# Kernel optimization log

Measured on AMD Instinct MI355X. Metric: run time of the kernel, lower is better.

## Reference

```python
import jax, jax.numpy as jnp
import numpy as np
import math

B, HO, WO, MO, NID, NOBJ = 8, 152, 272, 128, 537, 64
EMB_SCALE = math.sqrt(2.0) * math.log(NID - 1)

# ---------- host-side target construction (faithful CenterNet/FairMOT assignment) ----------

def gaussian_radius(det_size, min_overlap=0.7):
    height, width = det_size
    b1 = height + width
    c1 = width * height * (1 - min_overlap) / (1 + min_overlap)
    r1 = (b1 + math.sqrt(max(b1 * b1 - 4 * c1, 0.0))) / 2
    b2 = 2 * (height + width)
    c2 = (1 - min_overlap) * width * height
    r2 = (b2 + math.sqrt(max(b2 * b2 - 16 * c2, 0.0))) / 2
    a3 = 4 * min_overlap
    b3 = -2 * min_overlap * (height + width)
    c3 = (min_overlap - 1) * width * height
    r3 = (b3 + math.sqrt(max(b3 * b3 - 4 * a3 * c3, 0.0))) / 2
    return min(r1, r2, r3)

def gaussian2D(shape, sigma=1.0):
    m, n = [(s - 1.0) / 2.0 for s in shape]
    y, x = np.ogrid[-m:m + 1, -n:n + 1]
    h = np.exp(-(x * x + y * y) / (2 * sigma * sigma))
    h[h < np.finfo(h.dtype).eps * h.max()] = 0
    return h

def draw_umich_gaussian(heatmap, center, radius, k=1):
    diameter = 2 * radius + 1
    gaussian = gaussian2D((diameter, diameter), sigma=diameter / 6.0)
    x, y = int(center[0]), int(center[1])
    height, width = heatmap.shape
    left, right = min(x, radius), min(width - x, radius + 1)
    top, bottom = min(y, radius), min(height - y, radius + 1)
    mh = heatmap[y - top:y + bottom, x - left:x + right]
    mg = gaussian[radius - top:radius + bottom, radius - left:radius + right]
    if min(mg.shape) > 0 and min(mh.shape) > 0:
        np.maximum(mh, mg * k, out=mh)


def setup_inputs() -> dict:
    rng = np.random.default_rng(0)
    hm = np.zeros((B, 1, HO, WO), np.float32)
    wh = np.zeros((B, MO, 8), np.float32)
    v = np.zeros((B, MO), np.float32)
    ind = np.zeros((B, MO), np.int64)
    reg_mask = np.zeros((B, MO), np.int32)
    ids = np.zeros((B, MO), np.int64)
    for b in range(B):
        cx = rng.uniform(0.1, 0.9, NOBJ); cy = rng.uniform(0.1, 0.9, NOBJ)
        bw = rng.uniform(0.02, 0.15, NOBJ); bh = rng.uniform(0.05, 0.3, NOBJ)
        pid = rng.choice(NID, NOBJ, replace=False)
        vis = rng.uniform(0.3, 1.0, NOBJ)
        cx2 = np.clip(cx + rng.normal(0, 0.01, NOBJ), 0.05, 0.95)
        cy2 = np.clip(cy + rng.normal(0, 0.01, NOBJ), 0.05, 0.95)
        bw2 = bw * rng.uniform(0.9, 1.1, NOBJ); bh2 = bh * rng.uniform(0.9, 1.1, NOBJ)
        for k in range(NOBJ):
            x, y, w_, h_ = cx[k] * WO, cy[k] * HO, bw[k] * WO, bh[k] * HO
            ax0, ay0 = x - w_ / 2.0, y - h_ / 2.0
            ax1, ay1 = ax0 + w_, ay0 + h_
            xc, yc = float(np.clip(x, 0, WO - 1)), float(np.clip(y, 0, HO - 1))
            r = max(0, int(gaussian_radius((math.ceil(h_), math.ceil(w_)))))
            ctx, cty = int(xc), int(yc)
            draw_umich_gaussian(hm[b, 0], (ctx, cty), r)
            x2, y2, w2_, h2_ = cx2[k] * WO, cy2[k] * HO, bw2[k] * WO, bh2[k] * HO
            bx0, by0 = x2 - w2_ / 2.0, y2 - h2_ / 2.0
            bx1, by1 = bx0 + w2_, by0 + h2_
            if h_ > 0 and w_ > 0 and h2_ > 0 and w2_ > 0:
                ind[b, k] = cty * WO + ctx
                wh[b, k] = (ctx - ax0, ax1 - ctx, cty - ay0, ay1 - cty,
                            ctx - bx0, bx1 - ctx, cty - by0, by1 - cty)
                reg_mask[b, k] = 1
                ids[b, k] = pid[k]
                v[b, k] = vis[k]
    key = jax.random.key(0)
    ks = jax.random.split(key, 14)
    mk = lambda i, s: jax.random.normal(ks[i], s, dtype=jnp.float32)
    return {
        'classifications': mk(0, (B, 1, HO, WO)),
        'regressions': mk(1, (B, 8, HO, WO)),
        'viss': mk(2, (B, 1, HO, WO)),
        'identis_64': mk(3, (B, 64, HO, WO)),
        'identis_128': mk(4, (B, 128, HO, WO)),
        'identis_256': mk(5, (B, 256, HO, WO)),
        'identis_end': mk(6, (B, 128, HO, WO)),
        'hm': jnp.asarray(hm), 'wh': jnp.asarray(wh), 'v': jnp.asarray(v),
        'W64': mk(7, (NID, 64)) * 0.02, 'b64': jnp.zeros((NID,), jnp.float32),
        'W128': mk(8, (NID, 128)) * 0.02, 'b128': jnp.zeros((NID,), jnp.float32),
        'W256': mk(9, (NID, 256)) * 0.02, 'b256': jnp.zeros((NID,), jnp.float32),
        'Wend': mk(10, (NID, 128)) * 0.02, 'bend': jnp.zeros((NID,), jnp.float32),
        's_det': mk(11, (1,)), 's_id': mk(12, (1,)),
        'ind': jnp.asarray(ind), 'reg_mask': jnp.asarray(reg_mask), 'ids': jnp.asarray(ids),
    }

# ---------- jax loss math ----------

def _gather(feat, ind):
    # feat: [B,C,H,W] -> gathered [B,MO,C]
    b, c = feat.shape[0], feat.shape[1]
    f = feat.reshape(b, c, -1).transpose(0, 2, 1)  # [B,HW,C]
    return jnp.take_along_axis(f, ind[:, :, None], axis=1)


def _focal(pred, gt):
    # CenterNet focal loss, per image
    pos = (gt == 1.0).astype(pred.dtype)
    neg_w = (1.0 - gt) ** 4
    pos_l = jnp.log(pred) * (1.0 - pred) ** 2 * pos
    neg_l = jnp.log(1.0 - pred) * pred ** 2 * neg_w * (1.0 - pos)
    npos = pos.sum(axis=(1, 2, 3))
    pl, nl = pos_l.sum(axis=(1, 2, 3)), neg_l.sum(axis=(1, 2, 3))
    return jnp.where(npos > 0, -(pl + nl) / jnp.maximum(npos, 1.0), -nl)


def _reg_l1(pred_g, mask, target):
    # masked L1 normalized by expanded-mask sum (RegLoss)
    m = mask[:, :, None].astype(pred_g.dtype)
    num = (jnp.abs(pred_g - target) * m).sum(axis=(1, 2))
    den = mask.astype(pred_g.dtype).sum(axis=1) * pred_g.shape[-1] + 1e-4
    return num / den


def _id_loss(feat, ind, mask, ids, vw, Wc, bc):
    f = _gather(feat, ind)  # [B,MO,d]
    fn = EMB_SCALE * f / jnp.maximum(jnp.linalg.norm(f, axis=-1, keepdims=True), 1e-12)
    logits = jnp.einsum('bmd,nd->bmn', fn, Wc) + bc  # [B,MO,NID]
    logsm = jax.nn.log_softmax(logits, axis=-1)
    picked = jnp.take_along_axis(logsm, ids[:, :, None], axis=-1)[..., 0]  # [B,MO]
    mf = mask.astype(f.dtype)
    n = mf.sum(axis=1)
    return -(mf * vw * picked).sum(axis=1) / jnp.maximum(n, 1.0)


def reference(classifications, regressions, viss, identis_64, identis_128, identis_256,
              identis_end, hm, wh, v, W64, b64, W128, b128, W256, b256, Wend, bend,
              s_det, s_id, ind, reg_mask, ids):
    pred_cls = jnp.clip(jax.nn.sigmoid(classifications), 1e-4, 1.0 - 1e-4)
    pred_vis = jnp.clip(jax.nn.sigmoid(viss), 1e-4, 1.0 - 1e-4)

    cls_per = _focal(pred_cls, hm)                                    # [B]
    reg_per = _reg_l1(_gather(regressions, ind), reg_mask, wh)        # [B]
    vis_per = _reg_l1(_gather(pred_vis, ind), reg_mask, v[:, :, None])
    id_per = (_id_loss(identis_64, ind, reg_mask, ids, v, W64, b64)
              + _id_loss(identis_128, ind, reg_mask, ids, v, W128, b128)
              + _id_loss(identis_256, ind, reg_mask, ids, v, W256, b256)
              + _id_loss(identis_end, ind, reg_mask, ids, v, Wend, bend))

    return (cls_per.mean()[None], reg_per.mean()[None],
            vis_per.mean()[None], id_per.mean()[None])
```

## Files before the change

kernel.cpp:

```cpp
#include <hip/hip_runtime.h>
#include <math.h>

#define BB 8
#define HO_ 152
#define WO_ 272
#define HW (HO_*WO_)
#define MO_ 128
#define NID_ 537
#define EMB_SCALE 8.8871108f

#define WS_PL   0
#define WS_NL   8
#define WS_NP   16
#define WS_REG  24
#define WS_VIS  32
#define WS_ID   40
#define WS_FLOATS 48

__device__ __forceinline__ float block_sum(float v, float* red) {
#pragma unroll
    for (int off = 32; off > 0; off >>= 1) v += __shfl_down(v, off, 64);
    int w = threadIdx.x >> 6, lane = threadIdx.x & 63;
    __syncthreads();
    if (lane == 0) red[w] = v;
    __syncthreads();
    return red[0] + red[1] + red[2] + red[3];
}

__device__ __forceinline__ float block_max(float v, float* red) {
#pragma unroll
    for (int off = 32; off > 0; off >>= 1) v = fmaxf(v, __shfl_down(v, off, 64));
    int w = threadIdx.x >> 6, lane = threadIdx.x & 63;
    __syncthreads();
    if (lane == 0) red[w] = v;
    __syncthreads();
    return fmaxf(fmaxf(red[0], red[1]), fmaxf(red[2], red[3]));
}

__global__ __launch_bounds__(256) void focal_kernel(const float* __restrict__ cls,
                                                    const float* __restrict__ hm,
                                                    float* __restrict__ ws) {
    int b = blockIdx.y;
    const float* x = cls + (size_t)b * HW;
    const float* g = hm + (size_t)b * HW;
    float pl = 0.f, nl = 0.f, np = 0.f;
    for (int i = blockIdx.x * blockDim.x + threadIdx.x; i < HW; i += gridDim.x * blockDim.x) {
        float p = 1.f / (1.f + expf(-x[i]));
        p = fminf(fmaxf(p, 1e-4f), 1.f - 1e-4f);
        float gt = g[i];
        if (gt == 1.0f) {
            float q = 1.f - p;
            pl += logf(p) * q * q;
            np += 1.f;
        } else {
            float w = 1.f - gt; w *= w; w *= w;
            nl += logf(1.f - p) * p * p * w;
        }
    }
    __shared__ float red[8];
    pl = block_sum(pl, red);
    nl = block_sum(nl, red);
    np = block_sum(np, red);
    if (threadIdx.x == 0) {
        atomicAdd(&ws[WS_PL + b], pl);
        atomicAdd(&ws[WS_NL + b], nl);
        atomicAdd(&ws[WS_NP + b], np);
    }
}

__global__ __launch_bounds__(256) void row_kernel(
    const float* __restrict__ regs, const float* __restrict__ viss,
    const float* __restrict__ id64, const float* __restrict__ id128,
    const float* __restrict__ id256, const float* __restrict__ idend,
    const float* __restrict__ wh, const float* __restrict__ v,
    const float* __restrict__ W64, const float* __restrict__ b64,
    const float* __restrict__ W128, const float* __restrict__ b128,
    const float* __restrict__ W256, const float* __restrict__ b256,
    const float* __restrict__ Wend, const float* __restrict__ bend,
    const int* __restrict__ ind, const int* __restrict__ mask,
    const int* __restrict__ ids, float* __restrict__ ws) {

    const int row = blockIdx.x;
    const int b = row >> 7;
    if (mask[row] == 0) return;
    const int pos = ind[row];
    const int t = threadIdx.x;

    __shared__ float fLds[256];
    __shared__ float logits[NID_];
    __shared__ float red[8];

    if (t == 0) {
        float s = 0.f;
        for (int c = 0; c < 8; ++c) {
            float p = regs[((size_t)(b * 8 + c)) * HW + pos];
            s += fabsf(p - wh[row * 8 + c]);
        }
        atomicAdd(&ws[WS_REG + b], s);
        float x = viss[(size_t)b * HW + pos];
        float pv = 1.f / (1.f + expf(-x));
        pv = fminf(fmaxf(pv, 1e-4f), 1.f - 1e-4f);
        atomicAdd(&ws[WS_VIS + b], fabsf(pv - v[row]));
    }

    const float* F[4]  = {id64, id128, id256, idend};
    const float* W[4]  = {W64, W128, W256, Wend};
    const float* BS[4] = {b64, b128, b256, bend};
    const int    C4[4] = {64, 128, 256, 128};

    const int myid = ids[row];
    float picked_total = 0.f;

#pragma unroll 1
    for (int h = 0; h < 4; ++h) {
        const int C = C4[h];
        if (t < C) fLds[t] = F[h][((size_t)(b * C + t)) * HW + pos];
        __syncthreads();

        float sq = (t < C) ? fLds[t] * fLds[t] : 0.f;
        float sumsq = block_sum(sq, red);
        float scale = EMB_SCALE / fmaxf(sqrtf(sumsq), 1e-12f);

        const float4* f4 = (const float4*)fLds;
        const int nq = C >> 2;
        for (int n = t; n < NID_; n += 256) {
            const float4* wrow = (const float4*)(W[h] + (size_t)n * C);
            float dot = 0.f;
#pragma unroll 4
            for (int j = 0; j < nq; ++j) {
                float4 wv = wrow[j];
                float4 fv = f4[j];
                dot += wv.x * fv.x + wv.y * fv.y + wv.z * fv.z + wv.w * fv.w;
            }
            logits[n] = BS[h][n] + scale * dot;
        }
        __syncthreads();

        float lm = -INFINITY;
        for (int n = t; n < NID_; n += 256) lm = fmaxf(lm, logits[n]);
        float gmax = block_max(lm, red);

        float es = 0.f;
        for (int n = t; n < NID_; n += 256) es += expf(logits[n] - gmax);
        float ssum = block_sum(es, red);

        picked_total += logits[myid] - gmax - logf(ssum);
        __syncthreads();
    }

    if (t == 0) atomicAdd(&ws[WS_ID + b], v[row] * picked_total);
}

__global__ __launch_bounds__(256) void finalize_kernel(const int* __restrict__ mask,
                                                       const float* __restrict__ ws,
                                                       float* __restrict__ out) {
    int t = threadIdx.x;
    __shared__ float per[4][BB];
    if (t < BB) {
        int b = t;
        float cnt = 0.f;
        for (int m = 0; m < MO_; ++m) cnt += (float)mask[b * MO_ + m];
        float pl = ws[WS_PL + b], nl = ws[WS_NL + b], np = ws[WS_NP + b];
        per[0][b] = (np > 0.f) ? -(pl + nl) / fmaxf(np, 1.f) : -nl;
        per[1][b] = ws[WS_REG + b] / (cnt * 8.f + 1e-4f);
        per[2][b] = ws[WS_VIS + b] / (cnt * 1.f + 1e-4f);
        per[3][b] = -ws[WS_ID + b] / fmaxf(cnt, 1.f);
    }
    __syncthreads();
    if (t < 4) {
        float s = 0.f;
        for (int b = 0; b < BB; ++b) s += per[t][b];
        out[t] = s / (float)BB;
    }
}

extern "C" void kernel_launch(void* const* d_in, const int* in_sizes, int n_in,
                              void* d_out, int out_size, void* d_ws, size_t ws_size,
                              hipStream_t stream) {
    const float* cls   = (const float*)d_in[0];
    const float* regs  = (const float*)d_in[1];
    const float* viss  = (const float*)d_in[2];
    const float* id64  = (const float*)d_in[3];
    const float* id128 = (const float*)d_in[4];
    const float* id256 = (const float*)d_in[5];
    const float* idend = (const float*)d_in[6];
    const float* hm    = (const float*)d_in[7];
    const float* wh    = (const float*)d_in[8];
    const float* v     = (const float*)d_in[9];
    const float* W64   = (const float*)d_in[10];
    const float* b64   = (const float*)d_in[11];
    const float* W128  = (const float*)d_in[12];
    const float* b128  = (const float*)d_in[13];
    const float* W256  = (const float*)d_in[14];
    const float* b256  = (const float*)d_in[15];
    const float* Wend  = (const float*)d_in[16];
    const float* bend  = (const float*)d_in[17];
    const int* ind   = (const int*)d_in[20];
    const int* mask  = (const int*)d_in[21];
    const int* ids   = (const int*)d_in[22];

    float* ws  = (float*)d_ws;
    float* out = (float*)d_out;

    hipMemsetAsync(ws, 0, WS_FLOATS * sizeof(float), stream);

    focal_kernel<<<dim3(64, BB), 256, 0, stream>>>(cls, hm, ws);

    row_kernel<<<BB * MO_, 256, 0, stream>>>(
        regs, viss, id64, id128, id256, idend, wh, v,
        W64, b64, W128, b128, W256, b256, Wend, bend,
        ind, mask, ids, ws);

    finalize_kernel<<<1, 256, 0, stream>>>(mask, ws, out);
}
```

Before: 736.5 us.

## Split ID loss across heads and batch four rows per block for weight reuse

The monolithic per-row kernel becomes two kernels. One handles reg/vis L1 with one thread per row and warp reductions. The other puts each head on its own grid dimension and processes four rows per block, so every weight row loaded is reused across four dot products, and each wavefront runs its own softmax. The focal kernel is vectorised with float4 loads on a smaller grid. This cuts redundant W traffic and serial per-head syncs, at the cost of more LDS per block and one extra launch.

```diff
diff --git a/kernel.cpp b/kernel.cpp
--- a/kernel.cpp
+++ b/kernel.cpp
@@ -4,9 +4,10 @@
 #define BB 8
 #define HO_ 152
 #define WO_ 272
-#define HW (HO_*WO_)
+#define HW 41344
 #define MO_ 128
 #define NID_ 537
+#define NIDP 544
 #define EMB_SCALE 8.8871108f
 
 #define WS_PL   0
@@ -17,6 +18,17 @@
 #define WS_ID   40
 #define WS_FLOATS 48
 
+__device__ __forceinline__ float wsum(float v) {
+#pragma unroll
+    for (int o = 32; o > 0; o >>= 1) v += __shfl_xor(v, o, 64);
+    return v;
+}
+__device__ __forceinline__ float wmax(float v) {
+#pragma unroll
+    for (int o = 32; o > 0; o >>= 1) v = fmaxf(v, __shfl_xor(v, o, 64));
+    return v;
+}
+
 __device__ __forceinline__ float block_sum(float v, float* red) {
 #pragma unroll
     for (int off = 32; off > 0; off >>= 1) v += __shfl_down(v, off, 64);
@@ -25,39 +37,36 @@
     if (lane == 0) red[w] = v;
     __syncthreads();
     return red[0] + red[1] + red[2] + red[3];
-}
-
-__device__ __forceinline__ float block_max(float v, float* red) {
-#pragma unroll
-    for (int off = 32; off > 0; off >>= 1) v = fmaxf(v, __shfl_down(v, off, 64));
-    int w = threadIdx.x >> 6, lane = threadIdx.x & 63;
-    __syncthreads();
-    if (lane == 0) red[w] = v;
-    __syncthreads();
-    return fmaxf(fmaxf(red[0], red[1]), fmaxf(red[2], red[3]));
 }
 
 __global__ __launch_bounds__(256) void focal_kernel(const float* __restrict__ cls,
                                                     const float* __restrict__ hm,
                                                     float* __restrict__ ws) {
-    int b = blockIdx.y;
-    const float* x = cls + (size_t)b * HW;
-    const float* g = hm + (size_t)b * HW;
+    const int b = blockIdx.y;
+    const float4* x4 = (const float4*)(cls + (size_t)b * HW);
+    const float4* g4 = (const float4*)(hm + (size_t)b * HW);
     float pl = 0.f, nl = 0.f, np = 0.f;
-    for (int i = blockIdx.x * blockDim.x + threadIdx.x; i < HW; i += gridDim.x * blockDim.x) {
-        float p = 1.f / (1.f + expf(-x[i]));
-        p = fminf(fmaxf(p, 1e-4f), 1.f - 1e-4f);
-        float gt = g[i];
-        if (gt == 1.0f) {
-            float q = 1.f - p;
-            pl += logf(p) * q * q;
-            np += 1.f;
-        } else {
-            float w = 1.f - gt; w *= w; w *= w;
-            nl += logf(1.f - p) * p * p * w;
+    const int n4 = HW / 4;
+    for (int i = blockIdx.x * blockDim.x + threadIdx.x; i < n4; i += gridDim.x * blockDim.x) {
+        float4 xv = x4[i], gv = g4[i];
+        float xs[4] = {xv.x, xv.y, xv.z, xv.w};
+        float gs[4] = {gv.x, gv.y, gv.z, gv.w};
+#pragma unroll
+        for (int k = 0; k < 4; ++k) {
+            float p = 1.f / (1.f + expf(-xs[k]));
+            p = fminf(fmaxf(p, 1e-4f), 1.f - 1e-4f);
+            float gt = gs[k];
+            if (gt == 1.0f) {
+                float q = 1.f - p;
+                pl += logf(p) * q * q;
+                np += 1.f;
+            } else {
+                float w = 1.f - gt; w *= w; w *= w;
+                nl += logf(1.f - p) * p * p * w;
+            }
         }
     }
-    __shared__ float red[8];
+    __shared__ float red[4];
     pl = block_sum(pl, red);
     nl = block_sum(nl, red);
     np = block_sum(np, red);
@@ -68,87 +77,129 @@
     }
 }
 
-__global__ __launch_bounds__(256) void row_kernel(
+__global__ __launch_bounds__(256) void regvis_kernel(
     const float* __restrict__ regs, const float* __restrict__ viss,
+    const float* __restrict__ wh, const float* __restrict__ v,
+    const int* __restrict__ ind, const int* __restrict__ mask,
+    float* __restrict__ ws) {
+    const int row = blockIdx.x * 256 + threadIdx.x;
+    const int b = row >> 7;
+    const int l = threadIdx.x & 63;
+    float sreg = 0.f, svis = 0.f;
+    if (mask[row]) {
+        const int pos = ind[row];
+        const float* wr = wh + row * 8;
+        float s = 0.f;
+#pragma unroll
+        for (int c = 0; c < 8; ++c)
+            s += fabsf(regs[((size_t)(b * 8 + c)) * HW + pos] - wr[c]);
+        sreg = s;
+        float x = viss[(size_t)b * HW + pos];
+        float pv = 1.f / (1.f + expf(-x));
+        pv = fminf(fmaxf(pv, 1e-4f), 1.f - 1e-4f);
+        svis = fabsf(pv - v[row]);
+    }
+    sreg = wsum(sreg);
+    svis = wsum(svis);
+    if (l == 0) {
+        atomicAdd(&ws[WS_REG + b], sreg);
+        atomicAdd(&ws[WS_VIS + b], svis);
+    }
+}
+
+__global__ __launch_bounds__(256) void idloss_kernel(
     const float* __restrict__ id64, const float* __restrict__ id128,
     const float* __restrict__ id256, const float* __restrict__ idend,
-    const float* __restrict__ wh, const float* __restrict__ v,
     const float* __restrict__ W64, const float* __restrict__ b64,
     const float* __restrict__ W128, const float* __restrict__ b128,
     const float* __restrict__ W256, const float* __restrict__ b256,
     const float* __restrict__ Wend, const float* __restrict__ bend,
+    const float* __restrict__ v,
     const int* __restrict__ ind, const int* __restrict__ mask,
     const int* __restrict__ ids, float* __restrict__ ws) {
 
-    const int row = blockIdx.x;
-    const int b = row >> 7;
-    if (mask[row] == 0) return;
-    const int pos = ind[row];
+    const int g = blockIdx.x;
+    const int h = blockIdx.y;
     const int t = threadIdx.x;
-
-    __shared__ float fLds[256];
-    __shared__ float logits[NID_];
-    __shared__ float red[8];
-
-    if (t == 0) {
+    const int b = g >> 5;
+
+    __shared__ int   sInd[4], sMsk[4], sId[4];
+    __shared__ float sV[4], sSc[4];
+    __shared__ float fLds[4][256];
+    __shared__ float logits[4][NIDP];
+
+    if (t < 4) {
+        const int row = g * 4 + t;
+        sInd[t] = ind[row]; sMsk[t] = mask[row];
+        sId[t]  = ids[row]; sV[t]   = v[row];
+    }
+    __syncthreads();
+    if (!(sMsk[0] | sMsk[1] | sMsk[2] | sMsk[3])) return;
+
+    const float* F; const float* W; const float* Bs; int C;
+    switch (h) {
+        case 0: F = id64;  W = W64;  Bs = b64;  C = 64;  break;
+        case 1: F = id128; W = W128; Bs = b128; C = 128; break;
+        case 2: F = id256; W = W256; Bs = b256; C = 256; break;
+        default:F = idend; W = Wend; Bs = bend; C = 128; break;
+    }
+
+    if (t < C) {
+#pragma unroll
+        for (int r = 0; r < 4; ++r)
+            fLds[r][t] = F[((size_t)(b * C + t)) * HW + sInd[r]];
+    }
+    __syncthreads();
+
+    {
+        const int w = t >> 6, l = t & 63;
         float s = 0.f;
-        for (int c = 0; c < 8; ++c) {
-            float p = regs[((size_t)(b * 8 + c)) * HW + pos];
-            s += fabsf(p - wh[row * 8 + c]);
+        for (int j = l; j < C; j += 64) { float x = fLds[w][j]; s += x * x; }
+        s = wsum(s);
+        if (l == 0) sSc[w] = EMB_SCALE / fmaxf(sqrtf(s), 1e-12f);
+    }
+    __syncthreads();
+
+    const float s0 = sSc[0], s1 = sSc[1], s2 = sSc[2], s3 = sSc[3];
+    const float4* f0 = (const float4*)fLds[0];
+    const float4* f1 = (const float4*)fLds[1];
+    const float4* f2 = (const float4*)fLds[2];
+    const float4* f3 = (const float4*)fLds[3];
+    const int nq = C >> 2;
+
+    for (int n = t; n < NID_; n += 256) {
+        const float4* wr = (const float4*)(W + (size_t)n * C);
+        float d0 = 0.f, d1 = 0.f, d2 = 0.f, d3 = 0.f;
+#pragma unroll 4
+        for (int j = 0; j < nq; ++j) {
+            float4 wv = wr[j];
+            float4 a0 = f0[j], a1 = f1[j], a2 = f2[j], a3 = f3[j];
+            d0 += wv.x * a0.x + wv.y * a0.y + wv.z * a0.z + wv.w * a0.w;
+            d1 += wv.x * a1.x + wv.y * a1.y + wv.z * a1.z + wv.w * a1.w;
+            d2 += wv.x * a2.x + wv.y * a2.y + wv.z * a2.z + wv.w * a2.w;
+            d3 += wv.x * a3.x + wv.y * a3.y + wv.z * a3.z + wv.w * a3.w;
         }
-        atomicAdd(&ws[WS_REG + b], s);
-        float x = viss[(size_t)b * HW + pos];
-        float pv = 1.f / (1.f + expf(-x));
-        pv = fminf(fmaxf(pv, 1e-4f), 1.f - 1e-4f);
-        atomicAdd(&ws[WS_VIS + b], fabsf(pv - v[row]));
-    }
-
-    const float* F[4]  = {id64, id128, id256, idend};
-    const float* W[4]  = {W64, W128, W256, Wend};
-    const float* BS[4] = {b64, b128, b256, bend};
-    const int    C4[4] = {64, 128, 256, 128};
-
-    const int myid = ids[row];
-    float picked_total = 0.f;
-
-#pragma unroll 1
-    for (int h = 0; h < 4; ++h) {
-        const int C = C4[h];
-        if (t < C) fLds[t] = F[h][((size_t)(b * C + t)) * HW + pos];
-        __syncthreads();
-
-        float sq = (t < C) ? fLds[t] * fLds[t] : 0.f;
-        float sumsq = block_sum(sq, red);
-        float scale = EMB_SCALE / fmaxf(sqrtf(sumsq), 1e-12f);
-
-        const float4* f4 = (const float4*)fLds;
-        const int nq = C >> 2;
-        for (int n = t; n < NID_; n += 256) {
-            const float4* wrow = (const float4*)(W[h] + (size_t)n * C);
-            float dot = 0.f;
-#pragma unroll 4
-            for (int j = 0; j < nq; ++j) {
-                float4 wv = wrow[j];
-                float4 fv = f4[j];
-                dot += wv.x * fv.x + wv.y * fv.y + wv.z * fv.z + wv.w * fv.w;
-            }
-            logits[n] = BS[h][n] + scale * dot;
+        const float bb = Bs[n];
+        logits[0][n] = bb + s0 * d0;
+        logits[1][n] = bb + s1 * d1;
+        logits[2][n] = bb + s2 * d2;
+        logits[3][n] = bb + s3 * d3;
+    }
+    __syncthreads();
+
+    {
+        const int w = t >> 6, l = t & 63;
+        if (sMsk[w]) {
+            float m = -INFINITY;
+            for (int n = l; n < NID_; n += 64) m = fmaxf(m, logits[w][n]);
+            m = wmax(m);
+            float e = 0.f;
+            for (int n = l; n < NID_; n += 64) e += expf(logits[w][n] - m);
+            e = wsum(e);
+            if (l == 0)
+                atomicAdd(&ws[WS_ID + b], sV[w] * (logits[w][sId[w]] - m - logf(e)));
         }
-        __syncthreads();
-
-        float lm = -INFINITY;
-        for (int n = t; n < NID_; n += 256) lm = fmaxf(lm, logits[n]);
-        float gmax = block_max(lm, red);
-
-        float es = 0.f;
-        for (int n = t; n < NID_; n += 256) es += expf(logits[n] - gmax);
-        float ssum = block_sum(es, red);
-
-        picked_total += logits[myid] - gmax - logf(ssum);
-        __syncthreads();
-    }
-
-    if (t == 0) atomicAdd(&ws[WS_ID + b], v[row] * picked_total);
+    }
 }
 
 __global__ __launch_bounds__(256) void finalize_kernel(const int* __restrict__ mask,
@@ -204,12 +255,14 @@
 
     hipMemsetAsync(ws, 0, WS_FLOATS * sizeof(float), stream);
 
-    focal_kernel<<<dim3(64, BB), 256, 0, stream>>>(cls, hm, ws);
-
-    row_kernel<<<BB * MO_, 256, 0, stream>>>(
-        regs, viss, id64, id128, id256, idend, wh, v,
+    focal_kernel<<<dim3(16, BB), 256, 0, stream>>>(cls, hm, ws);
+
+    regvis_kernel<<<4, 256, 0, stream>>>(regs, viss, wh, v, ind, mask, ws);
+
+    idloss_kernel<<<dim3(256, 4), 256, 0, stream>>>(
+        id64, id128, id256, idend,
         W64, b64, W128, b128, W256, b256, Wend, bend,
-        ind, mask, ids, ws);
+        v, ind, mask, ids, ws);
 
     finalize_kernel<<<1, 256, 0, stream>>>(mask, ws, out);
 }
```

After: 648.2 us. 12.0% less time.
